# Optimization experiments

Hardware: AMD Instinct MI355X
Metric: run time of the kernel (lower is better)

The kernel has to match this reference:

```python
import jax, jax.numpy as jnp
import numpy as np

C = 1024
FACTOR = 4
C_INT = C * FACTOR


def setup_inputs() -> dict:
    key = jax.random.key(0)
    ks = jax.random.split(key, 6)
    act = jax.random.normal(ks[0], (4, 2048, C), dtype=jnp.float32)
    mask = jnp.ones((4, 2048), dtype=jnp.float32)
    # LayerNorm params
    ln_scale = jnp.ones((C,), dtype=jnp.float32)
    ln_bias = jnp.zeros((C,), dtype=jnp.float32)
    # Linear 1 (init='linear'): lecun-normal-ish
    w1 = jax.random.normal(ks[1], (C, C_INT), dtype=jnp.float32) / np.sqrt(C)
    b1 = jnp.zeros((C_INT,), dtype=jnp.float32)
    # Linear 2 (init='final' -> zeros in AF2; use small random so grads are nontrivial)
    w2 = jax.random.normal(ks[2], (C_INT, C), dtype=jnp.float32) * 0.02
    b2 = jnp.zeros((C,), dtype=jnp.float32)
    return {"act": act, "mask": mask, "ln_scale": ln_scale, "ln_bias": ln_bias,
            "w1": w1, "b1": b1, "w2": w2, "b2": b2}


def _layernorm(x, scale, bias, eps=1e-5):
    mu = jnp.mean(x, axis=-1, keepdims=True)
    var = jnp.mean(jnp.square(x - mu), axis=-1, keepdims=True)
    return (x - mu) * jax.lax.rsqrt(var + eps) * scale + bias


def reference(act, mask, ln_scale, ln_bias, w1, b1, w2, b2):
    # mask is accepted but unused, matching the original forward.
    x = _layernorm(act, ln_scale, ln_bias)
    h = jax.nn.relu(jnp.einsum('bsc,cf->bsf', x, w1) + b1)
    return jnp.einsum('bsf,fc->bsc', h, w2) + b2
```

## Files before the change

### kernel.cpp

```cpp
#include <hip/hip_runtime.h>
#include <hip/hip_bf16.h>
#include <cstdint>

typedef unsigned short u16;
typedef __bf16 bf16x8 __attribute__((ext_vector_type(8)));
typedef float floatx4 __attribute__((ext_vector_type(4)));

#define AS1 __attribute__((address_space(1)))
#define AS3 __attribute__((address_space(3)))

static __device__ __forceinline__ u16 f2bf(float f) {
    union { float f; unsigned int u; } v; v.f = f;
    unsigned int u = v.u;
    return (u16)((u + 0x7FFFu + ((u >> 16) & 1u)) >> 16);
}

__global__ __launch_bounds__(256)
void transpose_cvt(const float* __restrict__ in, u16* __restrict__ out,
                   int R, int Ccols)
{
    __shared__ float tile[32][33];
    const int tx = threadIdx.x;
    const int ty = threadIdx.y;
    const int c0 = blockIdx.x * 32;
    const int r0 = blockIdx.y * 32;
#pragma unroll
    for (int i = 0; i < 32; i += 8)
        tile[ty + i][tx] = in[(size_t)(r0 + ty + i) * Ccols + (c0 + tx)];
    __syncthreads();
#pragma unroll
    for (int i = 0; i < 32; i += 8)
        out[(size_t)(c0 + ty + i) * R + (r0 + tx)] = f2bf(tile[tx][ty + i]);
}

__global__ __launch_bounds__(256)
void ln_bf16(const float* __restrict__ act, const float* __restrict__ scale,
             const float* __restrict__ bias, u16* __restrict__ X)
{
    const int row = blockIdx.x;
    const int tid = threadIdx.x;
    const float4 v = ((const float4*)(act + (size_t)row * 1024))[tid];
    float s  = v.x + v.y + v.z + v.w;
    float ss = v.x * v.x + v.y * v.y + v.z * v.z + v.w * v.w;
#pragma unroll
    for (int off = 32; off > 0; off >>= 1) {
        s  += __shfl_xor(s, off, 64);
        ss += __shfl_xor(ss, off, 64);
    }
    __shared__ float red[8];
    const int wave = tid >> 6, lane = tid & 63;
    if (lane == 0) { red[wave] = s; red[4 + wave] = ss; }
    __syncthreads();
    s  = red[0] + red[1] + red[2] + red[3];
    ss = red[4] + red[5] + red[6] + red[7];
    const float mu  = s * (1.0f / 1024.0f);
    const float var = ss * (1.0f / 1024.0f) - mu * mu;
    const float rs  = rsqrtf(var + 1e-5f);
    const float4 sc = ((const float4*)scale)[tid];
    const float4 bi = ((const float4*)bias)[tid];
    ushort4 o;
    o.x = f2bf((v.x - mu) * rs * sc.x + bi.x);
    o.y = f2bf((v.y - mu) * rs * sc.y + bi.y);
    o.z = f2bf((v.z - mu) * rs * sc.z + bi.z);
    o.w = f2bf((v.w - mu) * rs * sc.w + bi.w);
    ((ushort4*)(X + (size_t)row * 1024))[tid] = o;
}

template <int BK, bool BF16_OUT, bool RELU>
__global__ __launch_bounds__(256)
void gemm_bt(const u16* __restrict__ A,
             const u16* __restrict__ Bt,
             const float* __restrict__ bias,
             void* __restrict__ Cout,
             int M, int N, int K)
{
    constexpr int SLOTS  = BK / 8;
    constexpr int RPI    = 64 / SLOTS;
    constexpr int IPW    = SLOTS / 2;
    constexpr int HALVES = BK / 32;

    __shared__ __align__(16) u16 Alds[128 * BK];
    __shared__ __align__(16) u16 Blds[128 * BK];

    const int tid  = threadIdx.x;
    const int wave = tid >> 6;
    const int lane = tid & 63;
    const int wm   = wave & 1;
    const int wn   = wave >> 1;
    const int quad = lane >> 4;
    const int l16  = lane & 15;

    const int bm = blockIdx.x;
    const int bn = blockIdx.y;

    const u16* Ag = A  + (size_t)bm * 128 * K;
    const u16* Bg = Bt + (size_t)bn * 128 * K;

    const int srow = lane / SLOTS;
    const int s_st = lane & (SLOTS - 1);
    const int s_g  = (SLOTS == 4) ? (s_st ^ ((srow >> 1) & 3))
                                  : (s_st ^ (srow & 7));
    const int scol = s_g * 8;

    const int rkey = (SLOTS == 4) ? ((l16 >> 1) & 3) : (l16 & 7);

    floatx4 acc[4][4];
#pragma unroll
    for (int i = 0; i < 4; ++i)
#pragma unroll
        for (int j = 0; j < 4; ++j)
            acc[i][j] = (floatx4){0.f, 0.f, 0.f, 0.f};

    for (int k0 = 0; k0 < K; k0 += BK) {
        __syncthreads();
#pragma unroll
        for (int r = 0; r < IPW; ++r) {
            const int chunk = wave * IPW + r;
            const int row = chunk * RPI + srow;
            __builtin_amdgcn_global_load_lds(
                (AS1 void*)(Ag + (size_t)row * K + k0 + scol),
                (AS3 void*)(&Alds[chunk * 512]), 16, 0, 0);
            __builtin_amdgcn_global_load_lds(
                (AS1 void*)(Bg + (size_t)row * K + k0 + scol),
                (AS3 void*)(&Blds[chunk * 512]), 16, 0, 0);
        }
        __syncthreads();

#pragma unroll
        for (int h = 0; h < HALVES; ++h) {
            const int slot = ((quad + 4 * h) ^ rkey) * 8;
            bf16x8 af[4], bfr[4];
#pragma unroll
            for (int mi = 0; mi < 4; ++mi) {
                const int arow = wm * 64 + mi * 16 + l16;
                af[mi] = *(const bf16x8*)(&Alds[arow * BK + slot]);
            }
#pragma unroll
            for (int ni = 0; ni < 4; ++ni) {
                const int brow = wn * 64 + ni * 16 + l16;
                bfr[ni] = *(const bf16x8*)(&Blds[brow * BK + slot]);
            }
#pragma unroll
            for (int mi = 0; mi < 4; ++mi)
#pragma unroll
                for (int ni = 0; ni < 4; ++ni)
                    acc[mi][ni] = __builtin_amdgcn_mfma_f32_16x16x32_bf16(
                        bfr[ni], af[mi], acc[mi][ni], 0, 0, 0);
        }
    }

    const int mbase = bm * 128 + wm * 64;
    const int nbase = bn * 128 + wn * 64;
#pragma unroll
    for (int mi = 0; mi < 4; ++mi) {
        const int m = mbase + mi * 16 + l16;
#pragma unroll
        for (int ni = 0; ni < 4; ++ni) {
            const int n0 = nbase + ni * 16 + quad * 4;
            const float4 bv = *(const float4*)&bias[n0];
            float v0 = acc[mi][ni][0] + bv.x;
            float v1 = acc[mi][ni][1] + bv.y;
            float v2 = acc[mi][ni][2] + bv.z;
            float v3 = acc[mi][ni][3] + bv.w;
            if (RELU) {
                v0 = fmaxf(v0, 0.f); v1 = fmaxf(v1, 0.f);
                v2 = fmaxf(v2, 0.f); v3 = fmaxf(v3, 0.f);
            }
            if (BF16_OUT) {
                ushort4 o = { f2bf(v0), f2bf(v1), f2bf(v2), f2bf(v3) };
                *(ushort4*)&((u16*)Cout)[(size_t)m * N + n0] = o;
            } else {
                float4 o = { v0, v1, v2, v3 };
                *(float4*)&((float*)Cout)[(size_t)m * N + n0] = o;
            }
        }
    }
}

extern "C" void kernel_launch(void* const* d_in, const int* in_sizes, int n_in,
                              void* d_out, int out_size, void* d_ws, size_t ws_size,
                              hipStream_t stream)
{
    const float* act      = (const float*)d_in[0];
    const float* ln_scale = (const float*)d_in[2];
    const float* ln_bias  = (const float*)d_in[3];
    const float* w1       = (const float*)d_in[4];
    const float* b1       = (const float*)d_in[5];
    const float* w2       = (const float*)d_in[6];
    const float* b2       = (const float*)d_in[7];
    float* out = (float*)d_out;

    const int M = 8192, C = 1024, CI = 4096;

    u16* X   = (u16*)d_ws;
    u16* W1t = X   + (size_t)M * C;
    u16* W2t = W1t + (size_t)CI * C;
    u16* H   = W2t + (size_t)C * CI;

    transpose_cvt<<<dim3(CI / 32, C / 32), dim3(32, 8), 0, stream>>>(w1, W1t, C, CI);
    transpose_cvt<<<dim3(C / 32, CI / 32), dim3(32, 8), 0, stream>>>(w2, W2t, CI, C);
    ln_bf16<<<M, 256, 0, stream>>>(act, ln_scale, ln_bias, X);
    gemm_bt<64, true, true><<<dim3(M / 128, CI / 128), 256, 0, stream>>>(
        X, W1t, b1, (void*)H, M, CI, C);
    gemm_bt<64, false, false><<<dim3(M / 128, C / 128), 256, 0, stream>>>(
        H, W2t, b2, (void*)out, M, C, CI);
}
```

Baseline: 279.3 us.

## Merge prep kernels and swizzle GEMM block order for L2 reuse

```diff
diff --git a/kernel.cpp b/kernel.cpp
--- a/kernel.cpp
+++ b/kernel.cpp
@@ -15,15 +15,14 @@
     return (u16)((u + 0x7FFFu + ((u >> 16) & 1u)) >> 16);
 }
 
-__global__ __launch_bounds__(256)
-void transpose_cvt(const float* __restrict__ in, u16* __restrict__ out,
-                   int R, int Ccols)
-{
-    __shared__ float tile[32][33];
-    const int tx = threadIdx.x;
-    const int ty = threadIdx.y;
-    const int c0 = blockIdx.x * 32;
-    const int r0 = blockIdx.y * 32;
+__device__ __forceinline__ void transpose_body(
+    const float* __restrict__ in, u16* __restrict__ out,
+    int R, int Ccols, int bx, int by, int tid, float (*tile)[33])
+{
+    const int tx = tid & 31;
+    const int ty = tid >> 5;
+    const int c0 = bx * 32;
+    const int r0 = by * 32;
 #pragma unroll
     for (int i = 0; i < 32; i += 8)
         tile[ty + i][tx] = in[(size_t)(r0 + ty + i) * Ccols + (c0 + tx)];
@@ -34,11 +33,25 @@
 }
 
 __global__ __launch_bounds__(256)
-void ln_bf16(const float* __restrict__ act, const float* __restrict__ scale,
-             const float* __restrict__ bias, u16* __restrict__ X)
-{
-    const int row = blockIdx.x;
+void prep(const float* __restrict__ w1, const float* __restrict__ w2,
+          const float* __restrict__ act, const float* __restrict__ ln_scale,
+          const float* __restrict__ ln_bias,
+          u16* __restrict__ W1t, u16* __restrict__ W2t, u16* __restrict__ X)
+{
+    __shared__ float smem[32][33];
+    const int id  = blockIdx.x;
     const int tid = threadIdx.x;
+
+    if (id < 4096) {
+        transpose_body(w1, W1t, 1024, 4096, id & 127, id >> 7, tid, smem);
+        return;
+    }
+    if (id < 8192) {
+        const int t = id - 4096;
+        transpose_body(w2, W2t, 4096, 1024, t & 31, t >> 5, tid, smem);
+        return;
+    }
+    const int row = id - 8192;
     const float4 v = ((const float4*)(act + (size_t)row * 1024))[tid];
     float s  = v.x + v.y + v.z + v.w;
     float ss = v.x * v.x + v.y * v.y + v.z * v.z + v.w * v.w;
@@ -47,7 +60,7 @@
         s  += __shfl_xor(s, off, 64);
         ss += __shfl_xor(ss, off, 64);
     }
-    __shared__ float red[8];
+    float* red = &smem[0][0];
     const int wave = tid >> 6, lane = tid & 63;
     if (lane == 0) { red[wave] = s; red[4 + wave] = ss; }
     __syncthreads();
@@ -56,8 +69,8 @@
     const float mu  = s * (1.0f / 1024.0f);
     const float var = ss * (1.0f / 1024.0f) - mu * mu;
     const float rs  = rsqrtf(var + 1e-5f);
-    const float4 sc = ((const float4*)scale)[tid];
-    const float4 bi = ((const float4*)bias)[tid];
+    const float4 sc = ((const float4*)ln_scale)[tid];
+    const float4 bi = ((const float4*)ln_bias)[tid];
     ushort4 o;
     o.x = f2bf((v.x - mu) * rs * sc.x + bi.x);
     o.y = f2bf((v.y - mu) * rs * sc.y + bi.y);
@@ -67,7 +80,7 @@
 }
 
 template <int BK, bool BF16_OUT, bool RELU>
-__global__ __launch_bounds__(256)
+__global__ __launch_bounds__(256, 5)
 void gemm_bt(const u16* __restrict__ A,
              const u16* __restrict__ Bt,
              const float* __restrict__ bias,
@@ -90,8 +103,12 @@
     const int quad = lane >> 4;
     const int l16  = lane & 15;
 
-    const int bm = blockIdx.x;
-    const int bn = blockIdx.y;
+    const int nbn = N >> 7;
+    const int id  = blockIdx.x;
+    const int grp = id / (8 * nbn);
+    const int rem = id - grp * 8 * nbn;
+    const int bm  = grp * 8 + (rem & 7);
+    const int bn  = rem >> 3;
 
     const u16* Ag = A  + (size_t)bm * 128 * K;
     const u16* Bg = Bt + (size_t)bn * 128 * K;
@@ -197,11 +214,9 @@
     u16* W2t = W1t + (size_t)CI * C;
     u16* H   = W2t + (size_t)C * CI;
 
-    transpose_cvt<<<dim3(CI / 32, C / 32), dim3(32, 8), 0, stream>>>(w1, W1t, C, CI);
-    transpose_cvt<<<dim3(C / 32, CI / 32), dim3(32, 8), 0, stream>>>(w2, W2t, CI, C);
-    ln_bf16<<<M, 256, 0, stream>>>(act, ln_scale, ln_bias, X);
-    gemm_bt<64, true, true><<<dim3(M / 128, CI / 128), 256, 0, stream>>>(
+    prep<<<16384, 256, 0, stream>>>(w1, w2, act, ln_scale, ln_bias, W1t, W2t, X);
+    gemm_bt<64, true, true><<<(M / 128) * (CI / 128), 256, 0, stream>>>(
         X, W1t, b1, (void*)H, M, CI, C);
-    gemm_bt<64, false, false><<<dim3(M / 128, C / 128), 256, 0, stream>>>(
+    gemm_bt<64, false, false><<<(M / 128) * (C / 128), 256, 0, stream>>>(
         H, W2t, b2, (void*)out, M, C, CI);
 }
```

Result: slower. 511.7 us (+83.2%).
